# Kernel tuning notes

Hardware: AMD Instinct MI355X
Metric: run time of the kernel (lower is better)

## Reference

```python
import jax, jax.numpy as jnp
import numpy as np

# dims per init_kwargs / input_specs
B, C, H, W = 8, 256, 56, 56
K = 3            # kernel_size
S = 1            # stride
D = 1            # dilation
HEAD = 1
MID = int(C * 0.2)   # se_ratio bottleneck = 51
GAIN = float(np.sqrt(2.0))  # calculate_gain('relu')


def setup_inputs() -> dict:
    key = jax.random.key(0)
    ks = jax.random.split(key, 6)
    sc = 0.05
    return {
        "x": jax.random.normal(ks[0], (B, C, H, W), jnp.float32),
        # channel branch: 1x1 convs stored as dense matrices
        "w1": jax.random.normal(ks[1], (MID, C), jnp.float32) * sc,
        "b1": jnp.zeros((MID,), jnp.float32),
        "w2": jax.random.normal(ks[2], (C * K * K, MID), jnp.float32) * sc,
        "b2": jnp.zeros((C * K * K,), jnp.float32),
        # spatial branch: 1x1 conv c -> head*k^2
        "ws": jax.random.normal(ks[3], (HEAD * K * K, C), jnp.float32) * sc,
        "bs": jnp.zeros((HEAD * K * K,), jnp.float32),
        # FilterNorm running_std parameter (channel branch): randn * gain/k
        "fn_std": jax.random.normal(ks[4], (C * K * K,), jnp.float32) * (GAIN / K),
    }


def _ddf_mul(x, cf, sf):
    """Decoupled dynamic filter, 'mul' combine.
    x: (B,C,H,W), cf: (B,C,K,K) channel filter, sf: (B,K*K,Ho,Wo) spatial filter.
    out[b,c,i,j] = sum_{u,v} x[b,c, i*S+(u-(K-1)/2)*D, j*S+(v-(K-1)/2)*D] * cf[b,c,u,v] * sf[b,u*K+v,i,j]
    Accumulate over the K*K taps to avoid materializing the unfolded tensor."""
    p = D * (K - 1) // 2
    xp = jnp.pad(x, ((0, 0), (0, 0), (p, p), (p, p)))
    Ho, Wo = H // S, W // S
    out = jnp.zeros((B, C, Ho, Wo), x.dtype)
    for u in range(K):
        for v in range(K):
            patch = xp[:, :, u * D:u * D + S * Ho:S, v * D:v * D + S * Wo:S]
            out = out + patch * cf[:, :, u, v][:, :, None, None] * sf[:, u * K + v][:, None]
    return out


def reference(x, w1, b1, w2, b2, ws, bs, fn_std):
    # ---- channel branch: SE-style filter generation ----
    pooled = x.mean((2, 3))                                  # (B,C) global avg pool
    y = jax.nn.relu(pooled @ w1.T + b1)                      # (B,MID)
    y = (y @ w2.T + b2).reshape(B, C, K * K)                 # (B,C,K^2)
    # FilterNorm 'channel': normalize over K^2 (torch std -> ddof=1), learned std
    y = (y - y.mean(-1, keepdims=True)) / (y.std(-1, ddof=1, keepdims=True) + 1e-10)
    cf = (y.reshape(B, C * K * K) * fn_std).reshape(B, C, K, K)
    # ---- spatial branch: 1x1 conv (stride S) + FilterNorm 'spatial' ----
    xs = x[:, :, ::S, ::S]
    sf = jnp.einsum('bchw,nc->bnhw', xs, ws) + bs[None, :, None, None]  # (B,K^2,Ho,Wo)
    sf = sf.reshape(B, HEAD, K * K, H // S, W // S)
    sf = (sf - sf.mean(2, keepdims=True)) / (sf.std(2, ddof=1, keepdims=True) + 1e-10)
    sf = sf.reshape(B, HEAD * K * K, H // S, W // S) * (GAIN / K)
    # ---- fused per-pixel gather-multiply-reduce (head=1 -> no group reshape) ----
    return _ddf_mul(x, cf, sf)
```

## Files before the change

kernel.cpp:

```cpp
#include <hip/hip_runtime.h>
#include <math.h>

#define BB   8
#define CC   256
#define HH   56
#define WW   56
#define KK   3
#define MIDN 51
#define NTAP (KK*KK)
#define CKK  (CC*NTAP)
#define HW   (HH*WW)
#define NCH  8
#define CPC  (CC/NCH)
#define PBLK 13
#define NCPB 4
#define TILE 3364
#define XSTR 33

__global__ __launch_bounds__(256) void k_sfpool(const float* __restrict__ x,
                                                const float* __restrict__ ws,
                                                float* __restrict__ partial,
                                                float* __restrict__ poolpart) {
    int blk = blockIdx.x;
    int pb = blk % PBLK;
    int tmp = blk / PBLK;
    int chunk = tmp % NCH;
    int b = tmp / NCH;
    int t = threadIdx.x;
    __shared__ float xs[256 * XSTR];
    __shared__ float wss[NTAP][CPC];
    __shared__ float psum[8][CPC];
    for (int idx = t; idx < NTAP * CPC; idx += 256) {
        int n = idx / CPC, c = idx - n * CPC;
        wss[n][c] = ws[n * CC + chunk * CPC + c];
    }
    const float* xb = x + ((size_t)(b * CC + chunk * CPC)) * HW + pb * 256;
    bool act = (pb * 256 + t < HW);
    #pragma unroll 4
    for (int c = 0; c < CPC; ++c) {
        float v = act ? xb[(size_t)c * HW + t] : 0.f;
        xs[t * XSTR + c] = v;
    }
    __syncthreads();
    {
        int c = t & 31, seg = t >> 5;
        float s = 0.f;
        #pragma unroll 8
        for (int i = 0; i < 32; ++i) s += xs[(seg * 32 + i) * XSTR + c];
        psum[seg][c] = s;
    }
    float acc[NTAP];
    #pragma unroll
    for (int n = 0; n < NTAP; ++n) acc[n] = 0.f;
    #pragma unroll 4
    for (int c = 0; c < CPC; ++c) {
        float xv = xs[t * XSTR + c];
        #pragma unroll
        for (int n = 0; n < NTAP; ++n) acc[n] += xv * wss[n][c];
    }
    if (act) {
        float* pp = partial + ((size_t)((b * NCH + chunk) * NTAP)) * HW + pb * 256 + t;
        #pragma unroll
        for (int n = 0; n < NTAP; ++n) pp[(size_t)n * HW] = acc[n];
    }
    __syncthreads();
    if (t < CPC) {
        float tot = 0.f;
        #pragma unroll
        for (int seg = 0; seg < 8; ++seg) tot += psum[seg][t];
        poolpart[((size_t)((b * NCH + chunk) * PBLK + pb)) * CPC + t] = tot;
    }
}

#define MLPBLK (BB*NCH)
#define W2CHUNK (CPC*NTAP*MIDN)
__global__ __launch_bounds__(256) void k_mlp_sfB(const float* __restrict__ poolpart,
                                                 const float* __restrict__ w1,
                                                 const float* __restrict__ b1,
                                                 const float* __restrict__ w2,
                                                 const float* __restrict__ b2,
                                                 const float* __restrict__ fn_std,
                                                 const float* __restrict__ partial,
                                                 const float* __restrict__ bs,
                                                 float* __restrict__ cf,
                                                 float* __restrict__ sf) {
    __shared__ float smem[W2CHUNK + 256 + 64 + CPC * NTAP];
    float* w2s = smem;
    float* ps  = smem + W2CHUNK;
    float* y1  = ps + 256;
    float* y2s = y1 + 64;
    int blk = blockIdx.x;
    int t = threadIdx.x;
    if (blk < MLPBLK) {
        int b = blk >> 3, chunk = blk & 7;
        int c0 = chunk * CPC;
        const float4* w2v = (const float4*)(w2 + (size_t)chunk * W2CHUNK);
        float4* w2s4 = (float4*)w2s;
        for (int i = t; i < W2CHUNK / 4; i += 256) w2s4[i] = w2v[i];
        {
            int chunkp = t >> 5, cl = t & 31;
            float s = 0.f;
            const float* pp = poolpart + ((size_t)(b * NCH + chunkp) * PBLK) * CPC + cl;
            #pragma unroll
            for (int pb = 0; pb < PBLK; ++pb) s += pp[pb * CPC];
            ps[t] = s * (1.0f / HW);
        }
        __syncthreads();
        if (t < MIDN) {
            float acc = b1[t];
            const float* wr = w1 + t * CC;
            for (int c2 = 0; c2 < CC; ++c2) acc += ps[c2] * wr[c2];
            y1[t] = fmaxf(acc, 0.f);
        }
        __syncthreads();
        #pragma unroll
        for (int base = 0; base < 512; base += 256) {
            int idx = base + t;
            if (idx < CPC * NTAP) {
                float acc = b2[c0 * NTAP + idx];
                const float* r = w2s + idx * MIDN;
                #pragma unroll 3
                for (int m = 0; m < MIDN; ++m) acc += y1[m] * r[m];
                y2s[idx] = acc;
            }
        }
        __syncthreads();
        if (t < CPC) {
            int c = c0 + t;
            float y2[NTAP];
            #pragma unroll
            for (int q = 0; q < NTAP; ++q) y2[q] = y2s[t * NTAP + q];
            float mean = 0.f;
            #pragma unroll
            for (int q = 0; q < NTAP; ++q) mean += y2[q];
            mean *= (1.f / NTAP);
            float var = 0.f;
            #pragma unroll
            for (int q = 0; q < NTAP; ++q) { float d = y2[q] - mean; var += d * d; }
            float inv = 1.f / (sqrtf(var * (1.f / (NTAP - 1))) + 1e-10f);
            #pragma unroll
            for (int q = 0; q < NTAP; ++q) {
                int idx = c * NTAP + q;
                cf[(size_t)b * CKK + idx] = (y2[q] - mean) * inv * fn_std[idx];
            }
        }
    } else {
        int sblk = blk - MLPBLK;
        int b = sblk / PBLK, pb = sblk % PBLK;
        int p = pb * 256 + t;
        if (p >= HW) return;
        float acc[NTAP];
        #pragma unroll
        for (int n = 0; n < NTAP; ++n) acc[n] = bs[n];
        const float* pp = partial + ((size_t)(b * NCH)) * NTAP * HW + p;
        for (int chunk = 0; chunk < NCH; ++chunk)
            #pragma unroll
            for (int n = 0; n < NTAP; ++n)
                acc[n] += pp[((size_t)(chunk * NTAP + n)) * HW];
        float mean = 0.f;
        #pragma unroll
        for (int n = 0; n < NTAP; ++n) mean += acc[n];
        mean *= (1.f / NTAP);
        float var = 0.f;
        #pragma unroll
        for (int n = 0; n < NTAP; ++n) { float d = acc[n] - mean; var += d * d; }
        float inv = 0.47140452079103173f /
                    (sqrtf(var * (1.f / (NTAP - 1))) + 1e-10f);
        #pragma unroll
        for (int n = 0; n < NTAP; ++n)
            sf[((size_t)(b * NTAP + n)) * HW + p] = (acc[n] - mean) * inv;
    }
}

__global__ __launch_bounds__(512) void k_ddf(const float* __restrict__ x,
                                             const float* __restrict__ cf,
                                             const float* __restrict__ sf,
                                             float* __restrict__ out) {
    int blk = blockIdx.x;
    int b = blk / (CC / NCPB), cg = blk % (CC / NCPB);
    int c0 = cg * NCPB;
    int t = threadIdx.x;
    __shared__ float xt[NCPB][TILE];
    for (int idx = t; idx < NCPB * TILE; idx += 512) ((float*)xt)[idx] = 0.f;
    __syncthreads();
    const float4* xp4 = (const float4*)(x + ((size_t)(b * CC + c0)) * HW);
    for (int i4 = t; i4 < NCPB * HW / 4; i4 += 512) {
        float4 v = xp4[i4];
        int k = i4 / (HW / 4);
        int rem4 = i4 - k * (HW / 4);
        int r = rem4 / (WW / 4);
        int col = 4 * (rem4 - r * (WW / 4));
        float* d = &xt[k][(r + 1) * 58 + col + 1];
        d[0] = v.x; d[1] = v.y; d[2] = v.z; d[3] = v.w;
    }
    float cf9[NCPB][NTAP];
    const float* cfp = cf + (size_t)b * CKK + c0 * NTAP;
    #pragma unroll
    for (int k = 0; k < NCPB; ++k)
        #pragma unroll
        for (int n = 0; n < NTAP; ++n) cf9[k][n] = cfp[k * NTAP + n];
    __syncthreads();
    const float* sfb = sf + (size_t)b * NTAP * HW;
    float* op = out + ((size_t)(b * CC + c0)) * HW;
    for (int idx = t; idx < HW; idx += 512) {
        int i = idx / WW, j = idx - i * WW;
        float s9[NTAP];
        #pragma unroll
        for (int n = 0; n < NTAP; ++n) s9[n] = sfb[(size_t)n * HW + idx];
        float acc[NCPB];
        #pragma unroll
        for (int k = 0; k < NCPB; ++k) acc[k] = 0.f;
        #pragma unroll
        for (int u = 0; u < KK; ++u)
            #pragma unroll
            for (int v = 0; v < KK; ++v) {
                int n = u * KK + v;
                int o = (i + u) * 58 + (j + v);
                #pragma unroll
                for (int k = 0; k < NCPB; ++k)
                    acc[k] += xt[k][o] * (cf9[k][n] * s9[n]);
            }
        #pragma unroll
        for (int k = 0; k < NCPB; ++k) op[(size_t)k * HW + idx] = acc[k];
    }
}

extern "C" void kernel_launch(void* const* d_in, const int* in_sizes, int n_in,
                              void* d_out, int out_size, void* d_ws, size_t ws_size,
                              hipStream_t stream) {
    const float* x      = (const float*)d_in[0];
    const float* w1     = (const float*)d_in[1];
    const float* b1     = (const float*)d_in[2];
    const float* w2     = (const float*)d_in[3];
    const float* b2     = (const float*)d_in[4];
    const float* ws     = (const float*)d_in[5];
    const float* bs     = (const float*)d_in[6];
    const float* fn_std = (const float*)d_in[7];
    float* out = (float*)d_out;

    float* wsf      = (float*)d_ws;
    float* cf       = wsf;
    float* sf       = cf + 18432;
    float* poolpart = sf + 225792;
    float* partial  = poolpart + 26624;

    k_sfpool<<<BB * NCH * PBLK, 256, 0, stream>>>(x, ws, partial, poolpart);
    k_mlp_sfB<<<MLPBLK + BB * PBLK, 256, 0, stream>>>(poolpart, w1, b1, w2, b2,
                                                      fn_std, partial, bs, cf, sf);
    k_ddf<<<BB * (CC / NCPB), 512, 0, stream>>>(x, cf, sf, out);
}
```

Measured before the change: 122.5 us.

## Vectorize ddf kernel: 4 pixels per thread with float4 LDS tile rows

Pads the shared-memory tile rows to 68 floats with a 4-float left margin, so both the global-to-LDS copy and the tap reads can use aligned float4 accesses. Each thread now computes four adjacent output pixels, reusing three float4 LDS loads per row across the horizontal taps. It also loads the spatial filter and stores the output as float4. The goals are fewer LDS and global transactions and more register reuse, at the cost of more registers per thread and only 196 active threads of 512 in the compute loop.

```diff
diff --git a/kernel.cpp b/kernel.cpp
--- a/kernel.cpp
+++ b/kernel.cpp
@@ -14,8 +14,9 @@
 #define CPC  (CC/NCH)
 #define PBLK 13
 #define NCPB 4
-#define TILE 3364
 #define XSTR 33
+#define TROW 68
+#define TPL  (58*TROW)
 
 __global__ __launch_bounds__(256) void k_sfpool(const float* __restrict__ x,
                                                 const float* __restrict__ ws,
@@ -180,8 +181,12 @@
     int b = blk / (CC / NCPB), cg = blk % (CC / NCPB);
     int c0 = cg * NCPB;
     int t = threadIdx.x;
-    __shared__ float xt[NCPB][TILE];
-    for (int idx = t; idx < NCPB * TILE; idx += 512) ((float*)xt)[idx] = 0.f;
+    __shared__ __align__(16) float xt[NCPB][TPL];
+    {
+        float4 z4 = make_float4(0.f, 0.f, 0.f, 0.f);
+        float4* xt4 = (float4*)xt;
+        for (int i4 = t; i4 < NCPB * TPL / 4; i4 += 512) xt4[i4] = z4;
+    }
     __syncthreads();
     const float4* xp4 = (const float4*)(x + ((size_t)(b * CC + c0)) * HW);
     for (int i4 = t; i4 < NCPB * HW / 4; i4 += 512) {
@@ -190,8 +195,7 @@
         int rem4 = i4 - k * (HW / 4);
         int r = rem4 / (WW / 4);
         int col = 4 * (rem4 - r * (WW / 4));
-        float* d = &xt[k][(r + 1) * 58 + col + 1];
-        d[0] = v.x; d[1] = v.y; d[2] = v.z; d[3] = v.w;
+        *(float4*)&xt[k][(r + 1) * TROW + col + 4] = v;
     }
     float cf9[NCPB][NTAP];
     const float* cfp = cf + (size_t)b * CKK + c0 * NTAP;
@@ -202,26 +206,41 @@
     __syncthreads();
     const float* sfb = sf + (size_t)b * NTAP * HW;
     float* op = out + ((size_t)(b * CC + c0)) * HW;
-    for (int idx = t; idx < HW; idx += 512) {
-        int i = idx / WW, j = idx - i * WW;
-        float s9[NTAP];
-        #pragma unroll
-        for (int n = 0; n < NTAP; ++n) s9[n] = sfb[(size_t)n * HW + idx];
-        float acc[NCPB];
-        #pragma unroll
-        for (int k = 0; k < NCPB; ++k) acc[k] = 0.f;
-        #pragma unroll
-        for (int u = 0; u < KK; ++u)
-            #pragma unroll
-            for (int v = 0; v < KK; ++v) {
-                int n = u * KK + v;
-                int o = (i + u) * 58 + (j + v);
-                #pragma unroll
-                for (int k = 0; k < NCPB; ++k)
-                    acc[k] += xt[k][o] * (cf9[k][n] * s9[n]);
+    for (int g = t; g < HW / 4; g += 512) {
+        int i = g / (WW / 4);
+        int j0 = 4 * (g - i * (WW / 4));
+        int pix = i * WW + j0;
+        float acc[NCPB][4];
+        #pragma unroll
+        for (int k = 0; k < NCPB; ++k) {
+            acc[k][0] = 0.f; acc[k][1] = 0.f; acc[k][2] = 0.f; acc[k][3] = 0.f;
+        }
+        #pragma unroll
+        for (int u = 0; u < KK; ++u) {
+            float4 s0 = *(const float4*)&sfb[(size_t)(u * 3 + 0) * HW + pix];
+            float4 s1 = *(const float4*)&sfb[(size_t)(u * 3 + 1) * HW + pix];
+            float4 s2 = *(const float4*)&sfb[(size_t)(u * 3 + 2) * HW + pix];
+            int base = (i + u) * TROW + j0;
+            #pragma unroll
+            for (int k = 0; k < NCPB; ++k) {
+                float4 A = *(const float4*)&xt[k][base];
+                float4 B = *(const float4*)&xt[k][base + 4];
+                float4 C = *(const float4*)&xt[k][base + 8];
+                float w0 = A.w, w1 = B.x, w2 = B.y, w3 = B.z, w4 = B.w, w5 = C.x;
+                float c_0 = cf9[k][u * 3 + 0];
+                float c_1 = cf9[k][u * 3 + 1];
+                float c_2 = cf9[k][u * 3 + 2];
+                acc[k][0] += w0 * (c_0 * s0.x) + w1 * (c_1 * s1.x) + w2 * (c_2 * s2.x);
+                acc[k][1] += w1 * (c_0 * s0.y) + w2 * (c_1 * s1.y) + w3 * (c_2 * s2.y);
+                acc[k][2] += w2 * (c_0 * s0.z) + w3 * (c_1 * s1.z) + w4 * (c_2 * s2.z);
+                acc[k][3] += w3 * (c_0 * s0.w) + w4 * (c_1 * s1.w) + w5 * (c_2 * s2.w);
             }
-        #pragma unroll
-        for (int k = 0; k < NCPB; ++k) op[(size_t)k * HW + idx] = acc[k];
+        }
+        #pragma unroll
+        for (int k = 0; k < NCPB; ++k) {
+            float4 o4 = make_float4(acc[k][0], acc[k][1], acc[k][2], acc[k][3]);
+            *(float4*)&op[(size_t)k * HW + pix] = o4;
+        }
     }
 }
 
```

After: 126.6 us. 3.4% more time.

## Reduce spatial-filter projection over all channels per pixel strip, drop partial buffer

Applied to the files above, without the earlier changes.

The spatial 1x1 conv is restructured so each block owns a 64-pixel strip and reduces over all 256 channels itself. Each block then normalizes sf directly instead of writing per-chunk partials that a second kernel summed. This removes the partial-sum round trip through global memory and the sf branch of the MLP kernel. In exchange there are fewer blocks (392 vs 832), which reduces parallelism, and poolpart grows to 49 strips per batch, which the MLP kernel must sum serially.

```diff
diff --git a/kernel.cpp b/kernel.cpp
--- a/kernel.cpp
+++ b/kernel.cpp
@@ -10,80 +10,95 @@
 #define NTAP (KK*KK)
 #define CKK  (CC*NTAP)
 #define HW   (HH*WW)
-#define NCH  8
-#define CPC  (CC/NCH)
-#define PBLK 13
+#define SPIX 64
+#define NSTR (HW/SPIX)
+#define CPR  128
+#define XSTR 65
 #define NCPB 4
 #define TILE 3364
-#define XSTR 33
-
-__global__ __launch_bounds__(256) void k_sfpool(const float* __restrict__ x,
-                                                const float* __restrict__ ws,
-                                                float* __restrict__ partial,
-                                                float* __restrict__ poolpart) {
+
+__global__ __launch_bounds__(256) void k_sf(const float* __restrict__ x,
+                                            const float* __restrict__ ws,
+                                            const float* __restrict__ bs,
+                                            float* __restrict__ sf,
+                                            float* __restrict__ poolpart) {
     int blk = blockIdx.x;
-    int pb = blk % PBLK;
-    int tmp = blk / PBLK;
-    int chunk = tmp % NCH;
-    int b = tmp / NCH;
+    int s = blk % NSTR;
+    int b = blk / NSTR;
     int t = threadIdx.x;
-    __shared__ float xs[256 * XSTR];
-    __shared__ float wss[NTAP][CPC];
-    __shared__ float psum[8][CPC];
-    for (int idx = t; idx < NTAP * CPC; idx += 256) {
-        int n = idx / CPC, c = idx - n * CPC;
-        wss[n][c] = ws[n * CC + chunk * CPC + c];
-    }
-    const float* xb = x + ((size_t)(b * CC + chunk * CPC)) * HW + pb * 256;
-    bool act = (pb * 256 + t < HW);
-    #pragma unroll 4
-    for (int c = 0; c < CPC; ++c) {
-        float v = act ? xb[(size_t)c * HW + t] : 0.f;
-        xs[t * XSTR + c] = v;
-    }
-    __syncthreads();
-    {
-        int c = t & 31, seg = t >> 5;
-        float s = 0.f;
-        #pragma unroll 8
-        for (int i = 0; i < 32; ++i) s += xs[(seg * 32 + i) * XSTR + c];
-        psum[seg][c] = s;
-    }
+    int p = t & 63;
+    int q = t >> 6;
+    __shared__ float xs[CPR * XSTR];
+    __shared__ float wss[NTAP][CC];
+    __shared__ float accq[NTAP * 4 * SPIX];
+    for (int idx = t; idx < NTAP * CC; idx += 256)
+        ((float*)wss)[idx] = ws[idx];
     float acc[NTAP];
     #pragma unroll
     for (int n = 0; n < NTAP; ++n) acc[n] = 0.f;
-    #pragma unroll 4
-    for (int c = 0; c < CPC; ++c) {
-        float xv = xs[t * XSTR + c];
-        #pragma unroll
-        for (int n = 0; n < NTAP; ++n) acc[n] += xv * wss[n][c];
-    }
-    if (act) {
-        float* pp = partial + ((size_t)((b * NCH + chunk) * NTAP)) * HW + pb * 256 + t;
-        #pragma unroll
-        for (int n = 0; n < NTAP; ++n) pp[(size_t)n * HW] = acc[n];
-    }
-    __syncthreads();
-    if (t < CPC) {
-        float tot = 0.f;
-        #pragma unroll
-        for (int seg = 0; seg < 8; ++seg) tot += psum[seg][t];
-        poolpart[((size_t)((b * NCH + chunk) * PBLK + pb)) * CPC + t] = tot;
-    }
-}
-
-#define MLPBLK (BB*NCH)
+    const float* xb = x + ((size_t)b * CC) * HW + s * SPIX;
+    #pragma unroll
+    for (int r = 0; r < 2; ++r) {
+        if (r) __syncthreads();
+        float vv[32];
+        #pragma unroll
+        for (int c = 0; c < 32; ++c)
+            vv[c] = xb[(size_t)(r * CPR + q * 32 + c) * HW + p];
+        #pragma unroll
+        for (int c = 0; c < 32; ++c)
+            xs[(q * 32 + c) * XSTR + p] = vv[c];
+        __syncthreads();
+        if (t < CPR) {
+            float sum = 0.f;
+            #pragma unroll 8
+            for (int pp = 0; pp < SPIX; ++pp) sum += xs[t * XSTR + pp];
+            poolpart[((size_t)(b * NSTR + s)) * CC + r * CPR + t] = sum;
+        }
+        #pragma unroll 4
+        for (int c = 0; c < 32; ++c) {
+            float xv = xs[(q * 32 + c) * XSTR + p];
+            #pragma unroll
+            for (int n = 0; n < NTAP; ++n)
+                acc[n] += xv * wss[n][r * CPR + q * 32 + c];
+        }
+    }
+    #pragma unroll
+    for (int n = 0; n < NTAP; ++n) accq[(n * 4 + q) * SPIX + p] = acc[n];
+    __syncthreads();
+    if (t < SPIX) {
+        float y[NTAP];
+        #pragma unroll
+        for (int n = 0; n < NTAP; ++n) {
+            float v = bs[n];
+            #pragma unroll
+            for (int qq = 0; qq < 4; ++qq) v += accq[(n * 4 + qq) * SPIX + t];
+            y[n] = v;
+        }
+        float mean = 0.f;
+        #pragma unroll
+        for (int n = 0; n < NTAP; ++n) mean += y[n];
+        mean *= (1.f / NTAP);
+        float var = 0.f;
+        #pragma unroll
+        for (int n = 0; n < NTAP; ++n) { float d = y[n] - mean; var += d * d; }
+        float inv = 0.47140452079103173f /
+                    (sqrtf(var * (1.f / (NTAP - 1))) + 1e-10f);
+        #pragma unroll
+        for (int n = 0; n < NTAP; ++n)
+            sf[((size_t)(b * NTAP + n)) * HW + s * SPIX + t] = (y[n] - mean) * inv;
+    }
+}
+
+#define MLPBLK (BB*8)
+#define CPC 32
 #define W2CHUNK (CPC*NTAP*MIDN)
-__global__ __launch_bounds__(256) void k_mlp_sfB(const float* __restrict__ poolpart,
-                                                 const float* __restrict__ w1,
-                                                 const float* __restrict__ b1,
-                                                 const float* __restrict__ w2,
-                                                 const float* __restrict__ b2,
-                                                 const float* __restrict__ fn_std,
-                                                 const float* __restrict__ partial,
-                                                 const float* __restrict__ bs,
-                                                 float* __restrict__ cf,
-                                                 float* __restrict__ sf) {
+__global__ __launch_bounds__(256) void k_mlp(const float* __restrict__ poolpart,
+                                             const float* __restrict__ w1,
+                                             const float* __restrict__ b1,
+                                             const float* __restrict__ w2,
+                                             const float* __restrict__ b2,
+                                             const float* __restrict__ fn_std,
+                                             float* __restrict__ cf) {
     __shared__ float smem[W2CHUNK + 256 + 64 + CPC * NTAP];
     float* w2s = smem;
     float* ps  = smem + W2CHUNK;
@@ -91,84 +106,55 @@
     float* y2s = y1 + 64;
     int blk = blockIdx.x;
     int t = threadIdx.x;
-    if (blk < MLPBLK) {
-        int b = blk >> 3, chunk = blk & 7;
-        int c0 = chunk * CPC;
-        const float4* w2v = (const float4*)(w2 + (size_t)chunk * W2CHUNK);
-        float4* w2s4 = (float4*)w2s;
-        for (int i = t; i < W2CHUNK / 4; i += 256) w2s4[i] = w2v[i];
-        {
-            int chunkp = t >> 5, cl = t & 31;
-            float s = 0.f;
-            const float* pp = poolpart + ((size_t)(b * NCH + chunkp) * PBLK) * CPC + cl;
-            #pragma unroll
-            for (int pb = 0; pb < PBLK; ++pb) s += pp[pb * CPC];
-            ps[t] = s * (1.0f / HW);
-        }
-        __syncthreads();
-        if (t < MIDN) {
-            float acc = b1[t];
-            const float* wr = w1 + t * CC;
-            for (int c2 = 0; c2 < CC; ++c2) acc += ps[c2] * wr[c2];
-            y1[t] = fmaxf(acc, 0.f);
-        }
-        __syncthreads();
-        #pragma unroll
-        for (int base = 0; base < 512; base += 256) {
-            int idx = base + t;
-            if (idx < CPC * NTAP) {
-                float acc = b2[c0 * NTAP + idx];
-                const float* r = w2s + idx * MIDN;
-                #pragma unroll 3
-                for (int m = 0; m < MIDN; ++m) acc += y1[m] * r[m];
-                y2s[idx] = acc;
-            }
-        }
-        __syncthreads();
-        if (t < CPC) {
-            int c = c0 + t;
-            float y2[NTAP];
-            #pragma unroll
-            for (int q = 0; q < NTAP; ++q) y2[q] = y2s[t * NTAP + q];
-            float mean = 0.f;
-            #pragma unroll
-            for (int q = 0; q < NTAP; ++q) mean += y2[q];
-            mean *= (1.f / NTAP);
-            float var = 0.f;
-            #pragma unroll
-            for (int q = 0; q < NTAP; ++q) { float d = y2[q] - mean; var += d * d; }
-            float inv = 1.f / (sqrtf(var * (1.f / (NTAP - 1))) + 1e-10f);
-            #pragma unroll
-            for (int q = 0; q < NTAP; ++q) {
-                int idx = c * NTAP + q;
-                cf[(size_t)b * CKK + idx] = (y2[q] - mean) * inv * fn_std[idx];
-            }
-        }
-    } else {
-        int sblk = blk - MLPBLK;
-        int b = sblk / PBLK, pb = sblk % PBLK;
-        int p = pb * 256 + t;
-        if (p >= HW) return;
-        float acc[NTAP];
-        #pragma unroll
-        for (int n = 0; n < NTAP; ++n) acc[n] = bs[n];
-        const float* pp = partial + ((size_t)(b * NCH)) * NTAP * HW + p;
-        for (int chunk = 0; chunk < NCH; ++chunk)
-            #pragma unroll
-            for (int n = 0; n < NTAP; ++n)
-                acc[n] += pp[((size_t)(chunk * NTAP + n)) * HW];
+    int b = blk >> 3, chunk = blk & 7;
+    int c0 = chunk * CPC;
+    const float4* w2v = (const float4*)(w2 + (size_t)chunk * W2CHUNK);
+    float4* w2s4 = (float4*)w2s;
+    for (int i = t; i < W2CHUNK / 4; i += 256) w2s4[i] = w2v[i];
+    {
+        float s = 0.f;
+        const float* pp = poolpart + ((size_t)b * NSTR) * CC + t;
+        for (int st = 0; st < NSTR; ++st) s += pp[(size_t)st * CC];
+        ps[t] = s * (1.0f / HW);
+    }
+    __syncthreads();
+    if (t < MIDN) {
+        float acc = b1[t];
+        const float* wr = w1 + t * CC;
+        for (int c2 = 0; c2 < CC; ++c2) acc += ps[c2] * wr[c2];
+        y1[t] = fmaxf(acc, 0.f);
+    }
+    __syncthreads();
+    #pragma unroll
+    for (int base = 0; base < 512; base += 256) {
+        int idx = base + t;
+        if (idx < CPC * NTAP) {
+            float acc = b2[c0 * NTAP + idx];
+            const float* r = w2s + idx * MIDN;
+            #pragma unroll 3
+            for (int m = 0; m < MIDN; ++m) acc += y1[m] * r[m];
+            y2s[idx] = acc;
+        }
+    }
+    __syncthreads();
+    if (t < CPC) {
+        int c = c0 + t;
+        float y2[NTAP];
+        #pragma unroll
+        for (int qq = 0; qq < NTAP; ++qq) y2[qq] = y2s[t * NTAP + qq];
         float mean = 0.f;
         #pragma unroll
-        for (int n = 0; n < NTAP; ++n) mean += acc[n];
+        for (int qq = 0; qq < NTAP; ++qq) mean += y2[qq];
         mean *= (1.f / NTAP);
         float var = 0.f;
         #pragma unroll
-        for (int n = 0; n < NTAP; ++n) { float d = acc[n] - mean; var += d * d; }
-        float inv = 0.47140452079103173f /
-                    (sqrtf(var * (1.f / (NTAP - 1))) + 1e-10f);
-        #pragma unroll
-        for (int n = 0; n < NTAP; ++n)
-            sf[((size_t)(b * NTAP + n)) * HW + p] = (acc[n] - mean) * inv;
+        for (int qq = 0; qq < NTAP; ++qq) { float d = y2[qq] - mean; var += d * d; }
+        float inv = 1.f / (sqrtf(var * (1.f / (NTAP - 1))) + 1e-10f);
+        #pragma unroll
+        for (int qq = 0; qq < NTAP; ++qq) {
+            int idx = c * NTAP + qq;
+            cf[(size_t)b * CKK + idx] = (y2[qq] - mean) * inv * fn_std[idx];
+        }
     }
 }
 
@@ -242,10 +228,8 @@
     float* cf       = wsf;
     float* sf       = cf + 18432;
     float* poolpart = sf + 225792;
-    float* partial  = poolpart + 26624;
-
-    k_sfpool<<<BB * NCH * PBLK, 256, 0, stream>>>(x, ws, partial, poolpart);
-    k_mlp_sfB<<<MLPBLK + BB * PBLK, 256, 0, stream>>>(poolpart, w1, b1, w2, b2,
-                                                      fn_std, partial, bs, cf, sf);
+
+    k_sf<<<BB * NSTR, 256, 0, stream>>>(x, ws, bs, sf, poolpart);
+    k_mlp<<<MLPBLK, 256, 0, stream>>>(poolpart, w1, b1, w2, b2, fn_std, cf);
     k_ddf<<<BB * (CC / NCPB), 512, 0, stream>>>(x, cf, sf, out);
 }
```

After: 118.4 us. 1.03x faster.
